# Performance work log

Hardware: AMD Instinct MI355X
Metric: run time of the kernel (lower is better)

The kernel has to match this reference:

```python
import jax, jax.numpy as jnp
import numpy as np

D_MODEL = 1024
NUM_HEADS = 16
HEAD_DIM = D_MODEL // NUM_HEADS


def setup_inputs() -> dict:
    key = jax.random.key(0)
    k_x, k_qw, k_qb, k_ow, k_ob = jax.random.split(key, 5)
    s = 1.0 / np.sqrt(D_MODEL)
    return {
        "x": jax.random.normal(k_x, (2, 2048, D_MODEL), dtype=jnp.float32),
        "qkv_w": jax.random.uniform(k_qw, (3 * D_MODEL, D_MODEL), jnp.float32, -s, s),
        "qkv_b": jax.random.uniform(k_qb, (3 * D_MODEL,), jnp.float32, -s, s),
        "out_w": jax.random.uniform(k_ow, (D_MODEL, D_MODEL), jnp.float32, -s, s),
        "out_b": jax.random.uniform(k_ob, (D_MODEL,), jnp.float32, -s, s),
    }


def reference(x, qkv_w, qkv_b, out_w, out_b):
    B, S, D = x.shape
    # fused QKV projection: [B,S,3D]
    qkv = jnp.einsum("bsd,ed->bse", x, qkv_w) + qkv_b
    # [B,S,H,3*hd] -> [B,H,S,3*hd]
    qkv = qkv.reshape(B, S, NUM_HEADS, 3 * HEAD_DIM).transpose(0, 2, 1, 3)
    q, k, v = jnp.split(qkv, 3, axis=-1)
    scale = 1.0 / jnp.sqrt(jnp.asarray(HEAD_DIM, x.dtype))
    scores = jnp.einsum("bhqd,bhkd->bhqk", q, k) * scale
    attn = jax.nn.softmax(scores, axis=-1)
    vals = jnp.einsum("bhqk,bhkd->bhqd", attn, v)
    vals = vals.transpose(0, 2, 1, 3).reshape(B, S, D)
    return jnp.einsum("bsd,ed->bse", vals, out_w) + out_b
```

## Files before the change

kernel.cpp:

```cpp
#include <hip/hip_runtime.h>
#include <stdint.h>


#define D_MODEL 1024
#define NUM_HEADS 16
#define HEAD_DIM 64
#define BATCH 2
#define SEQ 2048
#define M_TOT (BATCH * SEQ)
#define QKV_N (3 * D_MODEL)

typedef __attribute__((ext_vector_type(8))) short bf16x8;
typedef __attribute__((ext_vector_type(4))) short bf16x4;
typedef __attribute__((ext_vector_type(4))) float f32x4;
typedef __attribute__((ext_vector_type(4))) unsigned int u32x4;

__device__ __forceinline__ unsigned short f2bf(float f) {
    union { float f; unsigned int u; } v; v.f = f;
    unsigned int u = v.u;
    u += 0x7fffu + ((u >> 16) & 1u);
    return (unsigned short)(u >> 16);
}

__device__ __forceinline__ unsigned int exp2_bf16u(float x) {
    return (unsigned int)__builtin_fmaf(x, 128.0f, 16251.58f);
}

__device__ __forceinline__ unsigned int perm_pack(unsigned int hi, unsigned int lo) {
#if __has_builtin(__builtin_amdgcn_perm)
    return __builtin_amdgcn_perm(hi, lo, 0x05040100u);
#else
    return (lo & 0xFFFFu) | (hi << 16);
#endif
}

__device__ __forceinline__ void gld_lds16(const unsigned short* g,
                                          unsigned short* l) {
#if __has_builtin(__builtin_amdgcn_global_load_lds)
    __builtin_amdgcn_global_load_lds(
        (const __attribute__((address_space(1))) unsigned int*)g,
        (__attribute__((address_space(3))) unsigned int*)l, 16, 0, 0);
#else
    *(u32x4*)(l + (threadIdx.x & 63) * 8) = *(const u32x4*)g;
#endif
}

__global__ __launch_bounds__(256) void cvt_all(const float* __restrict__ x,
                                               const float* __restrict__ qw,
                                               const float* __restrict__ ow,
                                               unsigned short* __restrict__ xb,
                                               unsigned short* __restrict__ wqb,
                                               unsigned short* __restrict__ wob) {
    int i = blockIdx.x * 256 + threadIdx.x;
    const int N1 = M_TOT * D_MODEL / 8;
    const int N2 = N1 + QKV_N * D_MODEL / 8;
    const float* src; unsigned short* dst; int j;
    if (i < N1)      { src = x;  dst = xb;  j = i; }
    else if (i < N2) { src = qw; dst = wqb; j = i - N1; }
    else             { src = ow; dst = wob; j = i - N2; }
    const float4* s = (const float4*)src;
    float4 a = s[2 * j], b = s[2 * j + 1];
    u32x4 o;
    o.x = (unsigned int)f2bf(a.x) | ((unsigned int)f2bf(a.y) << 16);
    o.y = (unsigned int)f2bf(a.z) | ((unsigned int)f2bf(a.w) << 16);
    o.z = (unsigned int)f2bf(b.x) | ((unsigned int)f2bf(b.y) << 16);
    o.w = (unsigned int)f2bf(b.z) | ((unsigned int)f2bf(b.w) << 16);
    *(u32x4*)(dst + 8 * (size_t)j) = o;
}

__global__ __launch_bounds__(512, 2) void gemm_qkv(const unsigned short* __restrict__ xb,
                                                   const unsigned short* __restrict__ wb,
                                                   const float* __restrict__ bias,
                                                   unsigned short* __restrict__ qb,
                                                   unsigned short* __restrict__ kb,
                                                   unsigned short* __restrict__ vtb) {
    __shared__ __align__(16) unsigned short L[57344];

    const int tid = threadIdx.x;
    const int lane = tid & 63, wave = tid >> 6;
    const int quad = lane >> 4, l16 = lane & 15, l7 = l16 & 7;
    const int lrow = lane >> 3;
    const int sw = (lane & 7) ^ lrow;
    const int m0 = blockIdx.x * 256;
    const int n0 = blockIdx.y * 192;
    const int wmr = (wave >> 2) * 128;
    const int wn = (wave & 3) * 48;

    float biasr[3];
#pragma unroll
    for (int nt = 0; nt < 3; nt++) biasr[nt] = bias[n0 + wn + nt * 16 + l16];

    f32x4 acc[8][3];
#pragma unroll
    for (int m = 0; m < 8; m++)
#pragma unroll
        for (int nt = 0; nt < 3; nt++) acc[m][nt] = (f32x4)0.0f;

    auto stA = [&](int tt, int s, int b) {
        int R = s * 64 + wave * 8 + lrow;
        gld_lds16(xb + (size_t)(m0 + R) * D_MODEL + tt * 64 + sw * 8,
                  L + b * 16384 + (s * 64 + wave * 8) * 64);
    };
    auto stB = [&](int tt, int s, int b) {
        int R = s * 64 + wave * 8 + lrow;
        gld_lds16(wb + (size_t)(n0 + R) * D_MODEL + tt * 64 + sw * 8,
                  L + 32768 + b * 12288 + (s * 64 + wave * 8) * 64);
    };

    stB(0, 0, 0); stB(0, 1, 0); stB(0, 2, 0);
    stA(0, 0, 0); stA(0, 1, 0); stA(0, 2, 0); stA(0, 3, 0);

    const int NT = D_MODEL / 64;
    for (int t = 0; t < NT; ++t) {
        const int cb = t & 1, nb = cb ^ 1;
        const int tn = (t + 1 < NT) ? t + 1 : NT - 1;
        const unsigned short* Ac = L + cb * 16384;
        const unsigned short* Bc = L + 32768 + cb * 12288;
        bf16x8 bfr[3][2];

#pragma unroll
        for (int q = 0; q < 4; ++q) {
            if (q == 0) {
                asm volatile("s_waitcnt vmcnt(1)" ::: "memory");
                asm volatile("s_barrier" ::: "memory");
            } else if (q == 2) {
                asm volatile("s_waitcnt vmcnt(4)" ::: "memory");
                asm volatile("s_barrier" ::: "memory");
            }
            if (q == 0)      { stB(tn, 0, nb); stB(tn, 1, nb); }
            else if (q == 1) { stB(tn, 2, nb); stA(tn, 0, nb); }
            else if (q == 2) { stA(tn, 1, nb); stA(tn, 2, nb); }
            else             { stA(tn, 3, nb); }

            if (q == 0) {
#pragma unroll
                for (int nt = 0; nt < 3; nt++)
#pragma unroll
                    for (int ks = 0; ks < 2; ++ks)
                        bfr[nt][ks] = *(const bf16x8*)(
                            Bc + (wn + nt * 16 + l16) * 64 + ((ks * 4 + quad) ^ l7) * 8);
            }
            bf16x8 afr[2][2];
#pragma unroll
            for (int j = 0; j < 2; ++j)
#pragma unroll
                for (int ks = 0; ks < 2; ++ks)
                    afr[j][ks] = *(const bf16x8*)(
                        Ac + (wmr + (q * 2 + j) * 16 + l16) * 64 + ((ks * 4 + quad) ^ l7) * 8);

            __builtin_amdgcn_s_setprio(1);
#pragma unroll
            for (int j = 0; j < 2; ++j)
#pragma unroll
                for (int nt = 0; nt < 3; nt++)
#pragma unroll
                    for (int ks = 0; ks < 2; ++ks)
                        acc[q * 2 + j][nt] = __builtin_amdgcn_mfma_f32_16x16x32_bf16(
                            afr[j][ks], bfr[nt][ks], acc[q * 2 + j][nt], 0, 0, 0);
            __builtin_amdgcn_s_setprio(0);
        }
    }

    __syncthreads();

    const float QSCALE = 0.18033688011112042f;
#pragma unroll
    for (int nt = 0; nt < 3; nt++) {
        int colb = wn + nt * 16;
        int sec = colb >> 6;
        int c64 = (colb & 63) + l16;
        float bia = biasr[nt];
        if (sec < 2) {
            unsigned short* img = L + sec * 16384;
            float scl = sec ? 1.0f : QSCALE;
#pragma unroll
            for (int mt = 0; mt < 8; mt++)
#pragma unroll
                for (int r = 0; r < 4; r++) {
                    int row = wmr + mt * 16 + quad * 4 + r;
                    img[row * 64 + ((((c64 >> 3) ^ (row & 7)) << 3) | (c64 & 7))] =
                        f2bf((acc[mt][nt][r] + bia) * scl);
                }
        } else {
            unsigned short* img = L + 32768;
            int d = c64;
#pragma unroll
            for (int mt = 0; mt < 8; mt++) {
                int cs = wmr + mt * 16 + quad * 4;
                int sb = cs >> 6, c64s = cs & 63;
                unsigned short t4[4];
#pragma unroll
                for (int r = 0; r < 4; r++) t4[r] = f2bf(acc[mt][nt][r] + bia);
                *(uint64_t*)(img + (d * 4 + sb) * 64 +
                             ((((c64s >> 3) ^ (d & 7)) << 3) | (c64s & 7))) =
                    *(const uint64_t*)t4;
            }
        }
    }
    __syncthreads();

    const int bh = (m0 >> 11) * NUM_HEADS + blockIdx.y;
    const int sbase = m0 & 2047;
    const int g = lane & 7;
#pragma unroll
    for (int p = 0; p < 4; p++) {
        int rr = p * 64 + wave * 8 + (lane >> 3);
        u32x4 ch = *(const u32x4*)(L + rr * 64 + ((g ^ (rr & 7)) << 3));
        *(u32x4*)(qb + ((size_t)bh * SEQ + sbase + rr) * 64 + g * 8) = ch;
        ch = *(const u32x4*)(L + 16384 + rr * 64 + ((g ^ (rr & 7)) << 3));
        *(u32x4*)(kb + ((size_t)bh * SEQ + sbase + rr) * 64 + g * 8) = ch;
        int d = rr >> 2, sb = rr & 3;
        ch = *(const u32x4*)(L + 32768 + rr * 64 + ((g ^ (d & 7)) << 3));
        *(u32x4*)(vtb + ((size_t)bh * 64 + d) * SEQ + sbase + sb * 64 + g * 8) = ch;
    }
}

__global__ __launch_bounds__(256, 4) void attn(const unsigned short* __restrict__ qb,
                                               const unsigned short* __restrict__ kb,
                                               const unsigned short* __restrict__ vtb,
                                               unsigned short* __restrict__ vals) {
    __shared__ __align__(16) unsigned short Ks[2][64 * 64];
    __shared__ __align__(16) unsigned short VTs[2][64 * 64];

    const int tid = threadIdx.x;
    const int lane = tid & 63, wave = tid >> 6;
    const int quad = lane >> 4, l16 = lane & 15;
    const int l7 = l16 & 7;
    const int bh = blockIdx.x;
    const int q0 = blockIdx.y * 64;
    const unsigned short* qh = qb + (size_t)bh * SEQ * 64;
    const unsigned short* kh = kb + (size_t)bh * SEQ * 64;
    const unsigned short* vth = vtb + (size_t)bh * 64 * SEQ;
    const int wrow = wave * 16;

    bf16x8 aq[2];
#pragma unroll
    for (int ks = 0; ks < 2; ++ks)
        aq[ks] = *(const bf16x8*)(
            qh + (size_t)(q0 + wrow + l16) * 64 + ks * 32 + quad * 8);

    const int lrow = lane >> 3;
    const int sw = (lane & 7) ^ (lrow & 7);

    int cxl0 = ((0 * 4 + quad) ^ l7) * 8;
    int cxl1 = ((1 * 4 + quad) ^ l7) * 8;

    auto stage = [&](int t, int b) {
        int kt = t * 64;
#pragma unroll
        for (int i = 0; i < 2; ++i) {
            int R = wave * 16 + i * 8;
            int row = R + lrow;
            int krow = (row & 0x23) | ((row & 0x0C) << 1) | ((row & 0x10) >> 2);
            gld_lds16(kh + (size_t)(kt + krow) * 64 + sw * 8, &Ks[b][R * 64]);
            gld_lds16(vth + (size_t)row * SEQ + kt + sw * 8, &VTs[b][R * 64]);
        }
    };

    stage(0, 0);
    __syncthreads();

    f32x4 oacc[4];
    f32x4 lsum = (f32x4)0.0f;
#pragma unroll
    for (int nt = 0; nt < 4; nt++) oacc[nt] = (f32x4)0.0f;

    bf16x8 ones8;
#pragma unroll
    for (int j = 0; j < 8; j++) ones8[j] = (short)0x3F80;

    const int NR = SEQ / 64;
    for (int t = 0; t < NR; ++t) {
        const int cur = t & 1;
        if (t + 1 < NR) stage(t + 1, cur ^ 1);

        const unsigned short* Kc = Ks[cur];
        const unsigned short* Vc = VTs[cur];

        f32x4 sacc[4];
#pragma unroll
        for (int mk = 0; mk < 4; mk++) sacc[mk] = (f32x4)0.0f;
#pragma unroll
        for (int ks = 0; ks < 2; ++ks) {
            int cxl = ks ? cxl1 : cxl0;
            bf16x8 bk[4];
#pragma unroll
            for (int mk = 0; mk < 4; mk++)
                bk[mk] = *(const bf16x8*)(Kc + (mk * 16 + l16) * 64 + cxl);
#pragma unroll
            for (int mk = 0; mk < 4; mk++)
                sacc[mk] = __builtin_amdgcn_mfma_f32_16x16x32_bf16(
                    bk[mk], aq[ks], sacc[mk], 0, 0, 0);
        }

        bf16x4 pf[4];
#pragma unroll
        for (int mk = 0; mk < 4; mk++) {
            unsigned int u0 = exp2_bf16u(sacc[mk][0]);
            unsigned int u1 = exp2_bf16u(sacc[mk][1]);
            unsigned int u2 = exp2_bf16u(sacc[mk][2]);
            unsigned int u3 = exp2_bf16u(sacc[mk][3]);
            union { unsigned int u[2]; bf16x4 b; } cv;
            cv.u[0] = perm_pack(u1, u0);
            cv.u[1] = perm_pack(u3, u2);
            pf[mk] = cv.b;
        }

#pragma unroll
        for (int w = 0; w < 2; ++w) {
            bf16x8 ap = __builtin_shufflevector(
                pf[2 * w], pf[2 * w + 1], 0, 1, 2, 3, 4, 5, 6, 7);
            int cxl = w ? cxl1 : cxl0;
#pragma unroll
            for (int nt = 0; nt < 4; nt++) {
                bf16x8 bv = *(const bf16x8*)(Vc + (nt * 16 + l16) * 64 + cxl);
                oacc[nt] = __builtin_amdgcn_mfma_f32_16x16x32_bf16(
                    ap, bv, oacc[nt], 0, 0, 0);
            }
            lsum = __builtin_amdgcn_mfma_f32_16x16x32_bf16(
                ap, ones8, lsum, 0, 0, 0);
        }
        __syncthreads();
    }

    const int b = bh >> 4, h = bh & 15;
    f32x4 inv;
#pragma unroll
    for (int r = 0; r < 4; r++) inv[r] = 1.0f / lsum[r];
#pragma unroll
    for (int nt = 0; nt < 4; nt++) {
        int d = nt * 16 + l16;
#pragma unroll
        for (int r = 0; r < 4; r++) {
            int row = wrow + quad * 4 + r;
            float v = oacc[nt][r] * inv[r];
            vals[((size_t)(b * SEQ + q0 + row)) * D_MODEL + h * 64 + d] =
                f2bf(v);
        }
    }
}

__global__ __launch_bounds__(512, 2) void gemm_out(const unsigned short* __restrict__ vb,
                                                   const unsigned short* __restrict__ wb,
                                                   const float* __restrict__ bias,
                                                   float* __restrict__ out) {
    __shared__ __align__(16) unsigned short L[32768];

    const int tid = threadIdx.x;
    const int lane = tid & 63, wave = tid >> 6;
    const int quad = lane >> 4, l16 = lane & 15, l7 = l16 & 7;
    const int lrow = lane >> 3;
    const int sw = (lane & 7) ^ lrow;
    const int m0 = blockIdx.y * 128, n0 = blockIdx.x * 128;
    const int wm = (wave >> 2) * 64;
    const int wn = (wave & 3) * 32;

    float biasr[2];
#pragma unroll
    for (int nt = 0; nt < 2; nt++) biasr[nt] = bias[n0 + wn + nt * 16 + l16];

    f32x4 acc[4][2];
#pragma unroll
    for (int mt = 0; mt < 4; mt++)
#pragma unroll
        for (int nt = 0; nt < 2; nt++) acc[mt][nt] = (f32x4)0.0f;

    auto stA = [&](int tt, int s, int b) {
        int R = (wave >> 2) * 64 + s * 32 + (wave & 3) * 8;
        gld_lds16(vb + (size_t)(m0 + R + lrow) * D_MODEL + tt * 64 + sw * 8,
                  L + b * 8192 + R * 64);
    };
    auto stB = [&](int tt, int s, int b) {
        int R = s * 64 + wave * 8;
        gld_lds16(wb + (size_t)(n0 + R + lrow) * D_MODEL + tt * 64 + sw * 8,
                  L + 16384 + b * 8192 + R * 64);
    };

    stB(0, 0, 0); stB(0, 1, 0); stA(0, 0, 0); stA(0, 1, 0);

    const int NT = D_MODEL / 64;
    for (int t = 0; t < NT; ++t) {
        const int cb = t & 1, nb = cb ^ 1;
        const int tn = (t + 1 < NT) ? t + 1 : NT - 1;
        const unsigned short* Ac = L + cb * 8192;
        const unsigned short* Bc = L + 16384 + cb * 8192;
        bf16x8 bfr[2][2];

#pragma unroll
        for (int p = 0; p < 2; ++p) {
            if (p == 0) {
                asm volatile("s_waitcnt vmcnt(1)" ::: "memory");
                asm volatile("s_barrier" ::: "memory");
                stB(tn, 0, nb); stB(tn, 1, nb);
            } else {
                asm volatile("s_waitcnt vmcnt(2)" ::: "memory");
                asm volatile("s_barrier" ::: "memory");
                stA(tn, 0, nb); stA(tn, 1, nb);
            }

            if (p == 0) {
#pragma unroll
                for (int nt = 0; nt < 2; nt++)
#pragma unroll
                    for (int ks = 0; ks < 2; ++ks)
                        bfr[nt][ks] = *(const bf16x8*)(
                            Bc + (wn + nt * 16 + l16) * 64 + ((ks * 4 + quad) ^ l7) * 8);
            }
            bf16x8 afr[2][2];
#pragma unroll
            for (int j = 0; j < 2; ++j)
#pragma unroll
                for (int ks = 0; ks < 2; ++ks)
                    afr[j][ks] = *(const bf16x8*)(
                        Ac + (wm + (p * 2 + j) * 16 + l16) * 64 + ((ks * 4 + quad) ^ l7) * 8);

            __builtin_amdgcn_s_setprio(1);
#pragma unroll
            for (int j = 0; j < 2; ++j)
#pragma unroll
                for (int nt = 0; nt < 2; nt++)
#pragma unroll
                    for (int ks = 0; ks < 2; ++ks)
                        acc[p * 2 + j][nt] = __builtin_amdgcn_mfma_f32_16x16x32_bf16(
                            afr[j][ks], bfr[nt][ks], acc[p * 2 + j][nt], 0, 0, 0);
            __builtin_amdgcn_s_setprio(0);
        }
    }

#pragma unroll
    for (int mt = 0; mt < 4; mt++)
#pragma unroll
        for (int nt = 0; nt < 2; nt++) {
            int n = n0 + wn + nt * 16 + l16;
#pragma unroll
            for (int r = 0; r < 4; r++) {
                int m = m0 + wm + mt * 16 + quad * 4 + r;
                out[(size_t)m * D_MODEL + n] = acc[mt][nt][r] + biasr[nt];
            }
        }
}

extern "C" void kernel_launch(void* const* d_in, const int* in_sizes, int n_in,
                              void* d_out, int out_size, void* d_ws, size_t ws_size,
                              hipStream_t stream) {
    const float* x = (const float*)d_in[0];
    const float* qkv_w = (const float*)d_in[1];
    const float* qkv_b = (const float*)d_in[2];
    const float* out_w = (const float*)d_in[3];
    const float* out_b = (const float*)d_in[4];
    float* out = (float*)d_out;

    char* ws = (char*)d_ws;
    size_t off = 0;
    auto carve = [&](size_t bytes) -> void* {
        void* p = ws + off;
        off += (bytes + 255) & ~(size_t)255;
        return p;
    };
    unsigned short* xb  = (unsigned short*)carve((size_t)M_TOT * D_MODEL * 2);
    unsigned short* wqb = (unsigned short*)carve((size_t)QKV_N * D_MODEL * 2);
    unsigned short* wob = (unsigned short*)carve((size_t)D_MODEL * D_MODEL * 2);
    unsigned short* qbuf = (unsigned short*)carve((size_t)M_TOT * D_MODEL * 2);
    unsigned short* kbuf = (unsigned short*)carve((size_t)M_TOT * D_MODEL * 2);
    unsigned short* vtb  = (unsigned short*)carve((size_t)M_TOT * D_MODEL * 2);
    unsigned short* vals = xb;

    const int NCHUNK = (M_TOT + QKV_N + D_MODEL) * D_MODEL / 8;
    cvt_all<<<NCHUNK / 256, 256, 0, stream>>>(x, qkv_w, out_w, xb, wqb, wob);

    gemm_qkv<<<dim3(M_TOT / 256, QKV_N / 192), 512, 0, stream>>>(
        xb, wqb, qkv_b, qbuf, kbuf, vtb);

    attn<<<dim3(BATCH * NUM_HEADS, SEQ / 64), 256, 0, stream>>>(
        qbuf, kbuf, vtb, vals);

    gemm_out<<<dim3(D_MODEL / 128, M_TOT / 128), 512, 0, stream>>>(
        vals, wob, out_b, out);
}
```

Measured before the change: 170.5 us.

## Give each attention wave two 16-row query tiles and halve block size

The attention kernel now launches 128 threads (2 waves) per 64-query block instead of 256, and each wave handles 32 query rows as two 16-row MFMA tiles. Each K/V fragment read from LDS is reused across both query tiles, which halves LDS reads per MFMA, and each thread stages twice as many K/V rows. The cost is more accumulator registers per wave and fewer waves per block to hide latency, and the launch-bounds occupancy hint drops from 4 to 2.

```diff
diff --git a/kernel.cpp b/kernel.cpp
--- a/kernel.cpp
+++ b/kernel.cpp
@@ -215,7 +215,7 @@
     }
 }
 
-__global__ __launch_bounds__(256, 4) void attn(const unsigned short* __restrict__ qb,
+__global__ __launch_bounds__(128, 2) void attn(const unsigned short* __restrict__ qb,
                                                const unsigned short* __restrict__ kb,
                                                const unsigned short* __restrict__ vtb,
                                                unsigned short* __restrict__ vals) {
@@ -231,13 +231,15 @@
     const unsigned short* qh = qb + (size_t)bh * SEQ * 64;
     const unsigned short* kh = kb + (size_t)bh * SEQ * 64;
     const unsigned short* vth = vtb + (size_t)bh * 64 * SEQ;
-    const int wrow = wave * 16;
-
-    bf16x8 aq[2];
-#pragma unroll
-    for (int ks = 0; ks < 2; ++ks)
-        aq[ks] = *(const bf16x8*)(
-            qh + (size_t)(q0 + wrow + l16) * 64 + ks * 32 + quad * 8);
+    const int wrow = wave * 32;
+
+    bf16x8 aq[2][2];
+#pragma unroll
+    for (int nq = 0; nq < 2; nq++)
+#pragma unroll
+        for (int ks = 0; ks < 2; ++ks)
+            aq[nq][ks] = *(const bf16x8*)(
+                qh + (size_t)(q0 + wrow + nq * 16 + l16) * 64 + ks * 32 + quad * 8);
 
     const int lrow = lane >> 3;
     const int sw = (lane & 7) ^ (lrow & 7);
@@ -248,8 +250,8 @@
     auto stage = [&](int t, int b) {
         int kt = t * 64;
 #pragma unroll
-        for (int i = 0; i < 2; ++i) {
-            int R = wave * 16 + i * 8;
+        for (int i = 0; i < 4; ++i) {
+            int R = wave * 32 + i * 8;
             int row = R + lrow;
             int krow = (row & 0x23) | ((row & 0x0C) << 1) | ((row & 0x10) >> 2);
             gld_lds16(kh + (size_t)(kt + krow) * 64 + sw * 8, &Ks[b][R * 64]);
@@ -260,10 +262,14 @@
     stage(0, 0);
     __syncthreads();
 
-    f32x4 oacc[4];
-    f32x4 lsum = (f32x4)0.0f;
-#pragma unroll
-    for (int nt = 0; nt < 4; nt++) oacc[nt] = (f32x4)0.0f;
+    f32x4 oacc[2][4];
+    f32x4 lsum[2];
+#pragma unroll
+    for (int mt = 0; mt < 2; mt++) {
+        lsum[mt] = (f32x4)0.0f;
+#pragma unroll
+        for (int nt = 0; nt < 4; nt++) oacc[mt][nt] = (f32x4)0.0f;
+    }
 
     bf16x8 ones8;
 #pragma unroll
@@ -277,9 +283,11 @@
         const unsigned short* Kc = Ks[cur];
         const unsigned short* Vc = VTs[cur];
 
-        f32x4 sacc[4];
-#pragma unroll
-        for (int mk = 0; mk < 4; mk++) sacc[mk] = (f32x4)0.0f;
+        f32x4 sacc[4][2];
+#pragma unroll
+        for (int mk = 0; mk < 4; mk++)
+#pragma unroll
+            for (int nq = 0; nq < 2; nq++) sacc[mk][nq] = (f32x4)0.0f;
 #pragma unroll
         for (int ks = 0; ks < 2; ++ks) {
             int cxl = ks ? cxl1 : cxl0;
@@ -289,53 +297,66 @@
                 bk[mk] = *(const bf16x8*)(Kc + (mk * 16 + l16) * 64 + cxl);
 #pragma unroll
             for (int mk = 0; mk < 4; mk++)
-                sacc[mk] = __builtin_amdgcn_mfma_f32_16x16x32_bf16(
-                    bk[mk], aq[ks], sacc[mk], 0, 0, 0);
-        }
-
-        bf16x4 pf[4];
-#pragma unroll
-        for (int mk = 0; mk < 4; mk++) {
-            unsigned int u0 = exp2_bf16u(sacc[mk][0]);
-            unsigned int u1 = exp2_bf16u(sacc[mk][1]);
-            unsigned int u2 = exp2_bf16u(sacc[mk][2]);
-            unsigned int u3 = exp2_bf16u(sacc[mk][3]);
-            union { unsigned int u[2]; bf16x4 b; } cv;
-            cv.u[0] = perm_pack(u1, u0);
-            cv.u[1] = perm_pack(u3, u2);
-            pf[mk] = cv.b;
-        }
+#pragma unroll
+                for (int nq = 0; nq < 2; nq++)
+                    sacc[mk][nq] = __builtin_amdgcn_mfma_f32_16x16x32_bf16(
+                        bk[mk], aq[nq][ks], sacc[mk][nq], 0, 0, 0);
+        }
+
+        bf16x4 pf[4][2];
+#pragma unroll
+        for (int mk = 0; mk < 4; mk++)
+#pragma unroll
+            for (int nq = 0; nq < 2; nq++) {
+                unsigned int u0 = exp2_bf16u(sacc[mk][nq][0]);
+                unsigned int u1 = exp2_bf16u(sacc[mk][nq][1]);
+                unsigned int u2 = exp2_bf16u(sacc[mk][nq][2]);
+                unsigned int u3 = exp2_bf16u(sacc[mk][nq][3]);
+                union { unsigned int u[2]; bf16x4 b; } cv;
+                cv.u[0] = perm_pack(u1, u0);
+                cv.u[1] = perm_pack(u3, u2);
+                pf[mk][nq] = cv.b;
+            }
 
 #pragma unroll
         for (int w = 0; w < 2; ++w) {
-            bf16x8 ap = __builtin_shufflevector(
-                pf[2 * w], pf[2 * w + 1], 0, 1, 2, 3, 4, 5, 6, 7);
+            bf16x8 ap0 = __builtin_shufflevector(
+                pf[2 * w][0], pf[2 * w + 1][0], 0, 1, 2, 3, 4, 5, 6, 7);
+            bf16x8 ap1 = __builtin_shufflevector(
+                pf[2 * w][1], pf[2 * w + 1][1], 0, 1, 2, 3, 4, 5, 6, 7);
             int cxl = w ? cxl1 : cxl0;
 #pragma unroll
             for (int nt = 0; nt < 4; nt++) {
                 bf16x8 bv = *(const bf16x8*)(Vc + (nt * 16 + l16) * 64 + cxl);
-                oacc[nt] = __builtin_amdgcn_mfma_f32_16x16x32_bf16(
-                    ap, bv, oacc[nt], 0, 0, 0);
-            }
-            lsum = __builtin_amdgcn_mfma_f32_16x16x32_bf16(
-                ap, ones8, lsum, 0, 0, 0);
+                oacc[0][nt] = __builtin_amdgcn_mfma_f32_16x16x32_bf16(
+                    ap0, bv, oacc[0][nt], 0, 0, 0);
+                oacc[1][nt] = __builtin_amdgcn_mfma_f32_16x16x32_bf16(
+                    ap1, bv, oacc[1][nt], 0, 0, 0);
+            }
+            lsum[0] = __builtin_amdgcn_mfma_f32_16x16x32_bf16(
+                ap0, ones8, lsum[0], 0, 0, 0);
+            lsum[1] = __builtin_amdgcn_mfma_f32_16x16x32_bf16(
+                ap1, ones8, lsum[1], 0, 0, 0);
         }
         __syncthreads();
     }
 
     const int b = bh >> 4, h = bh & 15;
-    f32x4 inv;
-#pragma unroll
-    for (int r = 0; r < 4; r++) inv[r] = 1.0f / lsum[r];
-#pragma unroll
-    for (int nt = 0; nt < 4; nt++) {
-        int d = nt * 16 + l16;
-#pragma unroll
-        for (int r = 0; r < 4; r++) {
-            int row = wrow + quad * 4 + r;
-            float v = oacc[nt][r] * inv[r];
-            vals[((size_t)(b * SEQ + q0 + row)) * D_MODEL + h * 64 + d] =
-                f2bf(v);
+#pragma unroll
+    for (int mt = 0; mt < 2; mt++) {
+        f32x4 inv;
+#pragma unroll
+        for (int r = 0; r < 4; r++) inv[r] = 1.0f / lsum[mt][r];
+#pragma unroll
+        for (int nt = 0; nt < 4; nt++) {
+            int d = nt * 16 + l16;
+#pragma unroll
+            for (int r = 0; r < 4; r++) {
+                int row = wrow + mt * 16 + quad * 4 + r;
+                float v = oacc[mt][nt][r] * inv[r];
+                vals[((size_t)(b * SEQ + q0 + row)) * D_MODEL + h * 64 + d] =
+                    f2bf(v);
+            }
         }
     }
 }
@@ -471,7 +492,7 @@
     gemm_qkv<<<dim3(M_TOT / 256, QKV_N / 192), 512, 0, stream>>>(
         xb, wqb, qkv_b, qbuf, kbuf, vtb);
 
-    attn<<<dim3(BATCH * NUM_HEADS, SEQ / 64), 256, 0, stream>>>(
+    attn<<<dim3(BATCH * NUM_HEADS, SEQ / 64), 128, 0, stream>>>(
         qbuf, kbuf, vtb, vals);
 
     gemm_out<<<dim3(D_MODEL / 128, M_TOT / 128), 512, 0, stream>>>(
```

After: 176.1 us. 3.3% more time.

## Fuse all four stages into one persistent cooperative kernel with grid syncs

Applied to the files above, without the earlier changes.

Replaces the four launches (convert, QKV GEMM, attention, output GEMM) with a single cooperative kernel of 256 blocks of 512 threads that runs each phase in turn, separated by grid.sync. The aim is to remove launch gaps and tail effects between kernels. In exchange, each phase is now tied to a fixed 256-block grid: attention runs two 256-thread units per block over two passes, and the GEMMs are remapped onto that grid. Grid-wide barriers add their own cost, and occupancy is limited to what fits co-resident.

```diff
diff --git a/kernel.cpp b/kernel.cpp
--- a/kernel.cpp
+++ b/kernel.cpp
@@ -1,5 +1,8 @@
 #include <hip/hip_runtime.h>
+#include <hip/hip_cooperative_groups.h>
 #include <stdint.h>
+
+namespace cg = cooperative_groups;
 
 
 #define D_MODEL 1024
@@ -45,399 +48,407 @@
 #endif
 }
 
-__global__ __launch_bounds__(256) void cvt_all(const float* __restrict__ x,
-                                               const float* __restrict__ qw,
-                                               const float* __restrict__ ow,
-                                               unsigned short* __restrict__ xb,
-                                               unsigned short* __restrict__ wqb,
-                                               unsigned short* __restrict__ wob) {
-    int i = blockIdx.x * 256 + threadIdx.x;
-    const int N1 = M_TOT * D_MODEL / 8;
-    const int N2 = N1 + QKV_N * D_MODEL / 8;
-    const float* src; unsigned short* dst; int j;
-    if (i < N1)      { src = x;  dst = xb;  j = i; }
-    else if (i < N2) { src = qw; dst = wqb; j = i - N1; }
-    else             { src = ow; dst = wob; j = i - N2; }
-    const float4* s = (const float4*)src;
-    float4 a = s[2 * j], b = s[2 * j + 1];
-    u32x4 o;
-    o.x = (unsigned int)f2bf(a.x) | ((unsigned int)f2bf(a.y) << 16);
-    o.y = (unsigned int)f2bf(a.z) | ((unsigned int)f2bf(a.w) << 16);
-    o.z = (unsigned int)f2bf(b.x) | ((unsigned int)f2bf(b.y) << 16);
-    o.w = (unsigned int)f2bf(b.z) | ((unsigned int)f2bf(b.w) << 16);
-    *(u32x4*)(dst + 8 * (size_t)j) = o;
-}
-
-__global__ __launch_bounds__(512, 2) void gemm_qkv(const unsigned short* __restrict__ xb,
-                                                   const unsigned short* __restrict__ wb,
-                                                   const float* __restrict__ bias,
-                                                   unsigned short* __restrict__ qb,
-                                                   unsigned short* __restrict__ kb,
-                                                   unsigned short* __restrict__ vtb) {
+__global__ __launch_bounds__(512, 2) void mha_fused(
+        const float* __restrict__ x, const float* __restrict__ qw,
+        const float* __restrict__ ow, const float* __restrict__ qkv_bias,
+        const float* __restrict__ out_bias,
+        unsigned short* __restrict__ xb, unsigned short* __restrict__ wqb,
+        unsigned short* __restrict__ wob, unsigned short* __restrict__ qb,
+        unsigned short* __restrict__ kb, unsigned short* __restrict__ vtb,
+        float* __restrict__ out) {
     __shared__ __align__(16) unsigned short L[57344];
-
+    cg::grid_group grid = cg::this_grid();
+
+    const int b = blockIdx.x;
     const int tid = threadIdx.x;
-    const int lane = tid & 63, wave = tid >> 6;
-    const int quad = lane >> 4, l16 = lane & 15, l7 = l16 & 7;
-    const int lrow = lane >> 3;
-    const int sw = (lane & 7) ^ lrow;
-    const int m0 = blockIdx.x * 256;
-    const int n0 = blockIdx.y * 192;
-    const int wmr = (wave >> 2) * 128;
-    const int wn = (wave & 3) * 48;
-
-    float biasr[3];
-#pragma unroll
-    for (int nt = 0; nt < 3; nt++) biasr[nt] = bias[n0 + wn + nt * 16 + l16];
-
-    f32x4 acc[8][3];
-#pragma unroll
-    for (int m = 0; m < 8; m++)
-#pragma unroll
-        for (int nt = 0; nt < 3; nt++) acc[m][nt] = (f32x4)0.0f;
-
-    auto stA = [&](int tt, int s, int b) {
-        int R = s * 64 + wave * 8 + lrow;
-        gld_lds16(xb + (size_t)(m0 + R) * D_MODEL + tt * 64 + sw * 8,
-                  L + b * 16384 + (s * 64 + wave * 8) * 64);
-    };
-    auto stB = [&](int tt, int s, int b) {
-        int R = s * 64 + wave * 8 + lrow;
-        gld_lds16(wb + (size_t)(n0 + R) * D_MODEL + tt * 64 + sw * 8,
-                  L + 32768 + b * 12288 + (s * 64 + wave * 8) * 64);
-    };
-
-    stB(0, 0, 0); stB(0, 1, 0); stB(0, 2, 0);
-    stA(0, 0, 0); stA(0, 1, 0); stA(0, 2, 0); stA(0, 3, 0);
-
-    const int NT = D_MODEL / 64;
-    for (int t = 0; t < NT; ++t) {
-        const int cb = t & 1, nb = cb ^ 1;
-        const int tn = (t + 1 < NT) ? t + 1 : NT - 1;
-        const unsigned short* Ac = L + cb * 16384;
-        const unsigned short* Bc = L + 32768 + cb * 12288;
-        bf16x8 bfr[3][2];
-
-#pragma unroll
-        for (int q = 0; q < 4; ++q) {
-            if (q == 0) {
-                asm volatile("s_waitcnt vmcnt(1)" ::: "memory");
-                asm volatile("s_barrier" ::: "memory");
-            } else if (q == 2) {
-                asm volatile("s_waitcnt vmcnt(4)" ::: "memory");
-                asm volatile("s_barrier" ::: "memory");
-            }
-            if (q == 0)      { stB(tn, 0, nb); stB(tn, 1, nb); }
-            else if (q == 1) { stB(tn, 2, nb); stA(tn, 0, nb); }
-            else if (q == 2) { stA(tn, 1, nb); stA(tn, 2, nb); }
-            else             { stA(tn, 3, nb); }
-
-            if (q == 0) {
-#pragma unroll
-                for (int nt = 0; nt < 3; nt++)
+
+    {
+        const int N1 = M_TOT * D_MODEL / 8;
+        const int N2 = N1 + QKV_N * D_MODEL / 8;
+#pragma unroll
+        for (int it = 0; it < 8; ++it) {
+            int i = it * 131072 + b * 512 + tid;
+            const float* src; unsigned short* dst; int j;
+            if (i < N1)      { src = x;  dst = xb;  j = i; }
+            else if (i < N2) { src = qw; dst = wqb; j = i - N1; }
+            else             { src = ow; dst = wob; j = i - N2; }
+            const float4* s = (const float4*)src;
+            float4 a = s[2 * j], c = s[2 * j + 1];
+            u32x4 o;
+            o.x = (unsigned int)f2bf(a.x) | ((unsigned int)f2bf(a.y) << 16);
+            o.y = (unsigned int)f2bf(a.z) | ((unsigned int)f2bf(a.w) << 16);
+            o.z = (unsigned int)f2bf(c.x) | ((unsigned int)f2bf(c.y) << 16);
+            o.w = (unsigned int)f2bf(c.z) | ((unsigned int)f2bf(c.w) << 16);
+            *(u32x4*)(dst + 8 * (size_t)j) = o;
+        }
+    }
+    grid.sync();
+    asm volatile("s_waitcnt vmcnt(0) lgkmcnt(0)" ::: "memory");
+
+    {
+        const int lane = tid & 63, wave = tid >> 6;
+        const int quad = lane >> 4, l16 = lane & 15, l7 = l16 & 7;
+        const int lrow = lane >> 3;
+        const int sw = (lane & 7) ^ lrow;
+        const int m0 = (b & 15) * 256;
+        const int n0 = (b >> 4) * 192;
+        const int wmr = (wave >> 2) * 128;
+        const int wn = (wave & 3) * 48;
+
+        float biasr[3];
+#pragma unroll
+        for (int nt = 0; nt < 3; nt++) biasr[nt] = qkv_bias[n0 + wn + nt * 16 + l16];
+
+        f32x4 acc[8][3];
+#pragma unroll
+        for (int m = 0; m < 8; m++)
+#pragma unroll
+            for (int nt = 0; nt < 3; nt++) acc[m][nt] = (f32x4)0.0f;
+
+        auto stA = [&](int tt, int s, int bb) {
+            int R = s * 64 + wave * 8 + lrow;
+            gld_lds16(xb + (size_t)(m0 + R) * D_MODEL + tt * 64 + sw * 8,
+                      L + bb * 16384 + (s * 64 + wave * 8) * 64);
+        };
+        auto stB = [&](int tt, int s, int bb) {
+            int R = s * 64 + wave * 8 + lrow;
+            gld_lds16(wqb + (size_t)(n0 + R) * D_MODEL + tt * 64 + sw * 8,
+                      L + 32768 + bb * 12288 + (s * 64 + wave * 8) * 64);
+        };
+
+        stB(0, 0, 0); stB(0, 1, 0); stB(0, 2, 0);
+        stA(0, 0, 0); stA(0, 1, 0); stA(0, 2, 0); stA(0, 3, 0);
+
+        const int NT = D_MODEL / 64;
+        for (int t = 0; t < NT; ++t) {
+            const int cb = t & 1, nb = cb ^ 1;
+            const int tn = (t + 1 < NT) ? t + 1 : NT - 1;
+            const unsigned short* Ac = L + cb * 16384;
+            const unsigned short* Bc = L + 32768 + cb * 12288;
+            bf16x8 bfr[3][2];
+
+#pragma unroll
+            for (int q = 0; q < 4; ++q) {
+                if (q == 0) {
+                    asm volatile("s_waitcnt vmcnt(1)" ::: "memory");
+                    asm volatile("s_barrier" ::: "memory");
+                } else if (q == 2) {
+                    asm volatile("s_waitcnt vmcnt(4)" ::: "memory");
+                    asm volatile("s_barrier" ::: "memory");
+                }
+                if (q == 0)      { stB(tn, 0, nb); stB(tn, 1, nb); }
+                else if (q == 1) { stB(tn, 2, nb); stA(tn, 0, nb); }
+                else if (q == 2) { stA(tn, 1, nb); stA(tn, 2, nb); }
+                else             { stA(tn, 3, nb); }
+
+                if (q == 0) {
+#pragma unroll
+                    for (int nt = 0; nt < 3; nt++)
+#pragma unroll
+                        for (int ks = 0; ks < 2; ++ks)
+                            bfr[nt][ks] = *(const bf16x8*)(
+                                Bc + (wn + nt * 16 + l16) * 64 + ((ks * 4 + quad) ^ l7) * 8);
+                }
+                bf16x8 afr[2][2];
+#pragma unroll
+                for (int j = 0; j < 2; ++j)
 #pragma unroll
                     for (int ks = 0; ks < 2; ++ks)
-                        bfr[nt][ks] = *(const bf16x8*)(
-                            Bc + (wn + nt * 16 + l16) * 64 + ((ks * 4 + quad) ^ l7) * 8);
-            }
-            bf16x8 afr[2][2];
-#pragma unroll
-            for (int j = 0; j < 2; ++j)
-#pragma unroll
-                for (int ks = 0; ks < 2; ++ks)
-                    afr[j][ks] = *(const bf16x8*)(
-                        Ac + (wmr + (q * 2 + j) * 16 + l16) * 64 + ((ks * 4 + quad) ^ l7) * 8);
-
-            __builtin_amdgcn_s_setprio(1);
-#pragma unroll
-            for (int j = 0; j < 2; ++j)
-#pragma unroll
-                for (int nt = 0; nt < 3; nt++)
+                        afr[j][ks] = *(const bf16x8*)(
+                            Ac + (wmr + (q * 2 + j) * 16 + l16) * 64 + ((ks * 4 + quad) ^ l7) * 8);
+
+                __builtin_amdgcn_s_setprio(1);
+#pragma unroll
+                for (int j = 0; j < 2; ++j)
+#pragma unroll
+                    for (int nt = 0; nt < 3; nt++)
+#pragma unroll
+                        for (int ks = 0; ks < 2; ++ks)
+                            acc[q * 2 + j][nt] = __builtin_amdgcn_mfma_f32_16x16x32_bf16(
+                                afr[j][ks], bfr[nt][ks], acc[q * 2 + j][nt], 0, 0, 0);
+                __builtin_amdgcn_s_setprio(0);
+            }
+        }
+
+        __syncthreads();
+
+        const float QSCALE = 0.18033688011112042f;
+#pragma unroll
+        for (int nt = 0; nt < 3; nt++) {
+            int colb = wn + nt * 16;
+            int sec = colb >> 6;
+            int c64 = (colb & 63) + l16;
+            float bia = biasr[nt];
+            if (sec < 2) {
+                unsigned short* img = L + sec * 16384;
+                float scl = sec ? 1.0f : QSCALE;
+#pragma unroll
+                for (int mt = 0; mt < 8; mt++)
+#pragma unroll
+                    for (int r = 0; r < 4; r++) {
+                        int row = wmr + mt * 16 + quad * 4 + r;
+                        img[row * 64 + ((((c64 >> 3) ^ (row & 7)) << 3) | (c64 & 7))] =
+                            f2bf((acc[mt][nt][r] + bia) * scl);
+                    }
+            } else {
+                unsigned short* img = L + 32768;
+                int d = c64;
+#pragma unroll
+                for (int mt = 0; mt < 8; mt++) {
+                    int cs = wmr + mt * 16 + quad * 4;
+                    int sb = cs >> 6, c64s = cs & 63;
+                    unsigned short t4[4];
+#pragma unroll
+                    for (int r = 0; r < 4; r++) t4[r] = f2bf(acc[mt][nt][r] + bia);
+                    *(uint64_t*)(img + (d * 4 + sb) * 64 +
+                                 ((((c64s >> 3) ^ (d & 7)) << 3) | (c64s & 7))) =
+                        *(const uint64_t*)t4;
+                }
+            }
+        }
+        __syncthreads();
+
+        const int bh = (m0 >> 11) * NUM_HEADS + (b >> 4);
+        const int sbase = m0 & 2047;
+        const int g = lane & 7;
+#pragma unroll
+        for (int p = 0; p < 4; p++) {
+            int rr = p * 64 + wave * 8 + (lane >> 3);
+            u32x4 ch = *(const u32x4*)(L + rr * 64 + ((g ^ (rr & 7)) << 3));
+            *(u32x4*)(qb + ((size_t)bh * SEQ + sbase + rr) * 64 + g * 8) = ch;
+            ch = *(const u32x4*)(L + 16384 + rr * 64 + ((g ^ (rr & 7)) << 3));
+            *(u32x4*)(kb + ((size_t)bh * SEQ + sbase + rr) * 64 + g * 8) = ch;
+            int d = rr >> 2, sb = rr & 3;
+            ch = *(const u32x4*)(L + 32768 + rr * 64 + ((g ^ (d & 7)) << 3));
+            *(u32x4*)(vtb + ((size_t)bh * 64 + d) * SEQ + sbase + sb * 64 + g * 8) = ch;
+        }
+    }
+    grid.sync();
+    asm volatile("s_waitcnt vmcnt(0) lgkmcnt(0)" ::: "memory");
+
+    {
+        const int u = tid >> 8;
+        const int utid = tid & 255;
+        const int lane = utid & 63, wave = utid >> 6;
+        const int quad = lane >> 4, l16 = lane & 15;
+        const int l7 = l16 & 7;
+        const int bh = b & 31;
+        unsigned short* UB = L + u * 16384;
+        const unsigned short* qh = qb + (size_t)bh * SEQ * 64;
+        const unsigned short* kh = kb + (size_t)bh * SEQ * 64;
+        const unsigned short* vth = vtb + (size_t)bh * 64 * SEQ;
+        const int wrow = wave * 16;
+
+        const int lrow = lane >> 3;
+        const int sw = (lane & 7) ^ (lrow & 7);
+        int cxl0 = ((0 * 4 + quad) ^ l7) * 8;
+        int cxl1 = ((1 * 4 + quad) ^ l7) * 8;
+
+        unsigned short* vals = xb;
+
+        for (int pass = 0; pass < 2; ++pass) {
+            const int q0 = ((b >> 5) * 4 + pass * 2 + u) * 64;
+
+            bf16x8 aq[2];
+#pragma unroll
+            for (int ks = 0; ks < 2; ++ks)
+                aq[ks] = *(const bf16x8*)(
+                    qh + (size_t)(q0 + wrow + l16) * 64 + ks * 32 + quad * 8);
+
+            auto stage = [&](int t, int bsel) {
+                int kt = t * 64;
+#pragma unroll
+                for (int i = 0; i < 2; ++i) {
+                    int R = wave * 16 + i * 8;
+                    int row = R + lrow;
+                    int krow = (row & 0x23) | ((row & 0x0C) << 1) | ((row & 0x10) >> 2);
+                    gld_lds16(kh + (size_t)(kt + krow) * 64 + sw * 8,
+                              UB + bsel * 4096 + R * 64);
+                    gld_lds16(vth + (size_t)row * SEQ + kt + sw * 8,
+                              UB + 8192 + bsel * 4096 + R * 64);
+                }
+            };
+
+            stage(0, 0);
+            __syncthreads();
+
+            f32x4 oacc[4];
+            f32x4 lsum = (f32x4)0.0f;
+#pragma unroll
+            for (int nt = 0; nt < 4; nt++) oacc[nt] = (f32x4)0.0f;
+
+            bf16x8 ones8;
+#pragma unroll
+            for (int j = 0; j < 8; j++) ones8[j] = (short)0x3F80;
+
+            const int NR = SEQ / 64;
+            for (int t = 0; t < NR; ++t) {
+                const int cur = t & 1;
+                if (t + 1 < NR) stage(t + 1, cur ^ 1);
+
+                const unsigned short* Kc = UB + cur * 4096;
+                const unsigned short* Vc = UB + 8192 + cur * 4096;
+
+                f32x4 sacc[4];
+#pragma unroll
+                for (int mk = 0; mk < 4; mk++) sacc[mk] = (f32x4)0.0f;
+#pragma unroll
+                for (int ks = 0; ks < 2; ++ks) {
+                    int cxl = ks ? cxl1 : cxl0;
+                    bf16x8 bk[4];
+#pragma unroll
+                    for (int mk = 0; mk < 4; mk++)
+                        bk[mk] = *(const bf16x8*)(Kc + (mk * 16 + l16) * 64 + cxl);
+#pragma unroll
+                    for (int mk = 0; mk < 4; mk++)
+                        sacc[mk] = __builtin_amdgcn_mfma_f32_16x16x32_bf16(
+                            bk[mk], aq[ks], sacc[mk], 0, 0, 0);
+                }
+
+                bf16x4 pf[4];
+#pragma unroll
+                for (int mk = 0; mk < 4; mk++) {
+                    unsigned int u0 = exp2_bf16u(sacc[mk][0]);
+                    unsigned int u1 = exp2_bf16u(sacc[mk][1]);
+                    unsigned int u2 = exp2_bf16u(sacc[mk][2]);
+                    unsigned int u3 = exp2_bf16u(sacc[mk][3]);
+                    union { unsigned int uu[2]; bf16x4 bb; } cv;
+                    cv.uu[0] = perm_pack(u1, u0);
+                    cv.uu[1] = perm_pack(u3, u2);
+                    pf[mk] = cv.bb;
+                }
+
+#pragma unroll
+                for (int w = 0; w < 2; ++w) {
+                    bf16x8 ap = __builtin_shufflevector(
+                        pf[2 * w], pf[2 * w + 1], 0, 1, 2, 3, 4, 5, 6, 7);
+                    int cxl = w ? cxl1 : cxl0;
+#pragma unroll
+                    for (int nt = 0; nt < 4; nt++) {
+                        bf16x8 bv = *(const bf16x8*)(Vc + (nt * 16 + l16) * 64 + cxl);
+                        oacc[nt] = __builtin_amdgcn_mfma_f32_16x16x32_bf16(
+                            ap, bv, oacc[nt], 0, 0, 0);
+                    }
+                    lsum = __builtin_amdgcn_mfma_f32_16x16x32_bf16(
+                        ap, ones8, lsum, 0, 0, 0);
+                }
+                __syncthreads();
+            }
+
+            const int bb = bh >> 4, h = bh & 15;
+            f32x4 inv;
+#pragma unroll
+            for (int r = 0; r < 4; r++) inv[r] = 1.0f / lsum[r];
+#pragma unroll
+            for (int nt = 0; nt < 4; nt++) {
+                int d = nt * 16 + l16;
+#pragma unroll
+                for (int r = 0; r < 4; r++) {
+                    int row = wrow + quad * 4 + r;
+                    float v = oacc[nt][r] * inv[r];
+                    vals[((size_t)(bb * SEQ + q0 + row)) * D_MODEL + h * 64 + d] =
+                        f2bf(v);
+                }
+            }
+        }
+    }
+    grid.sync();
+    asm volatile("s_waitcnt vmcnt(0) lgkmcnt(0)" ::: "memory");
+
+    {
+        const unsigned short* vb = xb;
+        const int lane = tid & 63, wave = tid >> 6;
+        const int quad = lane >> 4, l16 = lane & 15, l7 = l16 & 7;
+        const int lrow = lane >> 3;
+        const int sw = (lane & 7) ^ lrow;
+        const int m0 = (b >> 3) * 128, n0 = (b & 7) * 128;
+        const int wm = (wave >> 2) * 64;
+        const int wn = (wave & 3) * 32;
+
+        float biasr[2];
+#pragma unroll
+        for (int nt = 0; nt < 2; nt++) biasr[nt] = out_bias[n0 + wn + nt * 16 + l16];
+
+        f32x4 acc[4][2];
+#pragma unroll
+        for (int mt = 0; mt < 4; mt++)
+#pragma unroll
+            for (int nt = 0; nt < 2; nt++) acc[mt][nt] = (f32x4)0.0f;
+
+        auto stA = [&](int tt, int s, int bb) {
+            int R = (wave >> 2) * 64 + s * 32 + (wave & 3) * 8;
+            gld_lds16(vb + (size_t)(m0 + R + lrow) * D_MODEL + tt * 64 + sw * 8,
+                      L + bb * 8192 + R * 64);
+        };
+        auto stB = [&](int tt, int s, int bb) {
+            int R = s * 64 + wave * 8;
+            gld_lds16(wob + (size_t)(n0 + R + lrow) * D_MODEL + tt * 64 + sw * 8,
+                      L + 16384 + bb * 8192 + R * 64);
+        };
+
+        stB(0, 0, 0); stB(0, 1, 0); stA(0, 0, 0); stA(0, 1, 0);
+
+        const int NT = D_MODEL / 64;
+        for (int t = 0; t < NT; ++t) {
+            const int cb = t & 1, nb = cb ^ 1;
+            const int tn = (t + 1 < NT) ? t + 1 : NT - 1;
+            const unsigned short* Ac = L + cb * 8192;
+            const unsigned short* Bc = L + 16384 + cb * 8192;
+            bf16x8 bfr[2][2];
+
+#pragma unroll
+            for (int p = 0; p < 2; ++p) {
+                if (p == 0) {
+                    asm volatile("s_waitcnt vmcnt(1)" ::: "memory");
+                    asm volatile("s_barrier" ::: "memory");
+                    stB(tn, 0, nb); stB(tn, 1, nb);
+                } else {
+                    asm volatile("s_waitcnt vmcnt(2)" ::: "memory");
+                    asm volatile("s_barrier" ::: "memory");
+                    stA(tn, 0, nb); stA(tn, 1, nb);
+                }
+
+                if (p == 0) {
+#pragma unroll
+                    for (int nt = 0; nt < 2; nt++)
+#pragma unroll
+                        for (int ks = 0; ks < 2; ++ks)
+                            bfr[nt][ks] = *(const bf16x8*)(
+                                Bc + (wn + nt * 16 + l16) * 64 + ((ks * 4 + quad) ^ l7) * 8);
+                }
+                bf16x8 afr[2][2];
+#pragma unroll
+                for (int j = 0; j < 2; ++j)
 #pragma unroll
                     for (int ks = 0; ks < 2; ++ks)
-                        acc[q * 2 + j][nt] = __builtin_amdgcn_mfma_f32_16x16x32_bf16(
-                            afr[j][ks], bfr[nt][ks], acc[q * 2 + j][nt], 0, 0, 0);
-            __builtin_amdgcn_s_setprio(0);
-        }
+                        afr[j][ks] = *(const bf16x8*)(
+                            Ac + (wm + (p * 2 + j) * 16 + l16) * 64 + ((ks * 4 + quad) ^ l7) * 8);
+
+                __builtin_amdgcn_s_setprio(1);
+#pragma unroll
+                for (int j = 0; j < 2; ++j)
+#pragma unroll
+                    for (int nt = 0; nt < 2; nt++)
+#pragma unroll
+                        for (int ks = 0; ks < 2; ++ks)
+                            acc[p * 2 + j][nt] = __builtin_amdgcn_mfma_f32_16x16x32_bf16(
+                                afr[j][ks], bfr[nt][ks], acc[p * 2 + j][nt], 0, 0, 0);
+                __builtin_amdgcn_s_setprio(0);
+            }
+        }
+
+#pragma unroll
+        for (int mt = 0; mt < 4; mt++)
+#pragma unroll
+            for (int nt = 0; nt < 2; nt++) {
+                int n = n0 + wn + nt * 16 + l16;
+#pragma unroll
+                for (int r = 0; r < 4; r++) {
+                    int m = m0 + wm + mt * 16 + quad * 4 + r;
+                    out[(size_t)m * D_MODEL + n] = acc[mt][nt][r] + biasr[nt];
+                }
+            }
     }
-
-    __syncthreads();
-
-    const float QSCALE = 0.18033688011112042f;
-#pragma unroll
-    for (int nt = 0; nt < 3; nt++) {
-        int colb = wn + nt * 16;
-        int sec = colb >> 6;
-        int c64 = (colb & 63) + l16;
-        float bia = biasr[nt];
-        if (sec < 2) {
-            unsigned short* img = L + sec * 16384;
-            float scl = sec ? 1.0f : QSCALE;
-#pragma unroll
-            for (int mt = 0; mt < 8; mt++)
-#pragma unroll
-                for (int r = 0; r < 4; r++) {
-                    int row = wmr + mt * 16 + quad * 4 + r;
-                    img[row * 64 + ((((c64 >> 3) ^ (row & 7)) << 3) | (c64 & 7))] =
-                        f2bf((acc[mt][nt][r] + bia) * scl);
-                }
-        } else {
-            unsigned short* img = L + 32768;
-            int d = c64;
-#pragma unroll
-            for (int mt = 0; mt < 8; mt++) {
-                int cs = wmr + mt * 16 + quad * 4;
-                int sb = cs >> 6, c64s = cs & 63;
-                unsigned short t4[4];
-#pragma unroll
-                for (int r = 0; r < 4; r++) t4[r] = f2bf(acc[mt][nt][r] + bia);
-                *(uint64_t*)(img + (d * 4 + sb) * 64 +
-                             ((((c64s >> 3) ^ (d & 7)) << 3) | (c64s & 7))) =
-                    *(const uint64_t*)t4;
-            }
-        }
-    }
-    __syncthreads();
-
-    const int bh = (m0 >> 11) * NUM_HEADS + blockIdx.y;
-    const int sbase = m0 & 2047;
-    const int g = lane & 7;
-#pragma unroll
-    for (int p = 0; p < 4; p++) {
-        int rr = p * 64 + wave * 8 + (lane >> 3);
-        u32x4 ch = *(const u32x4*)(L + rr * 64 + ((g ^ (rr & 7)) << 3));
-        *(u32x4*)(qb + ((size_t)bh * SEQ + sbase + rr) * 64 + g * 8) = ch;
-        ch = *(const u32x4*)(L + 16384 + rr * 64 + ((g ^ (rr & 7)) << 3));
-        *(u32x4*)(kb + ((size_t)bh * SEQ + sbase + rr) * 64 + g * 8) = ch;
-        int d = rr >> 2, sb = rr & 3;
-        ch = *(const u32x4*)(L + 32768 + rr * 64 + ((g ^ (d & 7)) << 3));
-        *(u32x4*)(vtb + ((size_t)bh * 64 + d) * SEQ + sbase + sb * 64 + g * 8) = ch;
-    }
-}
-
-__global__ __launch_bounds__(256, 4) void attn(const unsigned short* __restrict__ qb,
-                                               const unsigned short* __restrict__ kb,
-                                               const unsigned short* __restrict__ vtb,
-                                               unsigned short* __restrict__ vals) {
-    __shared__ __align__(16) unsigned short Ks[2][64 * 64];
-    __shared__ __align__(16) unsigned short VTs[2][64 * 64];
-
-    const int tid = threadIdx.x;
-    const int lane = tid & 63, wave = tid >> 6;
-    const int quad = lane >> 4, l16 = lane & 15;
-    const int l7 = l16 & 7;
-    const int bh = blockIdx.x;
-    const int q0 = blockIdx.y * 64;
-    const unsigned short* qh = qb + (size_t)bh * SEQ * 64;
-    const unsigned short* kh = kb + (size_t)bh * SEQ * 64;
-    const unsigned short* vth = vtb + (size_t)bh * 64 * SEQ;
-    const int wrow = wave * 16;
-
-    bf16x8 aq[2];
-#pragma unroll
-    for (int ks = 0; ks < 2; ++ks)
-        aq[ks] = *(const bf16x8*)(
-            qh + (size_t)(q0 + wrow + l16) * 64 + ks * 32 + quad * 8);
-
-    const int lrow = lane >> 3;
-    const int sw = (lane & 7) ^ (lrow & 7);
-
-    int cxl0 = ((0 * 4 + quad) ^ l7) * 8;
-    int cxl1 = ((1 * 4 + quad) ^ l7) * 8;
-
-    auto stage = [&](int t, int b) {
-        int kt = t * 64;
-#pragma unroll
-        for (int i = 0; i < 2; ++i) {
-            int R = wave * 16 + i * 8;
-            int row = R + lrow;
-            int krow = (row & 0x23) | ((row & 0x0C) << 1) | ((row & 0x10) >> 2);
-            gld_lds16(kh + (size_t)(kt + krow) * 64 + sw * 8, &Ks[b][R * 64]);
-            gld_lds16(vth + (size_t)row * SEQ + kt + sw * 8, &VTs[b][R * 64]);
-        }
-    };
-
-    stage(0, 0);
-    __syncthreads();
-
-    f32x4 oacc[4];
-    f32x4 lsum = (f32x4)0.0f;
-#pragma unroll
-    for (int nt = 0; nt < 4; nt++) oacc[nt] = (f32x4)0.0f;
-
-    bf16x8 ones8;
-#pragma unroll
-    for (int j = 0; j < 8; j++) ones8[j] = (short)0x3F80;
-
-    const int NR = SEQ / 64;
-    for (int t = 0; t < NR; ++t) {
-        const int cur = t & 1;
-        if (t + 1 < NR) stage(t + 1, cur ^ 1);
-
-        const unsigned short* Kc = Ks[cur];
-        const unsigned short* Vc = VTs[cur];
-
-        f32x4 sacc[4];
-#pragma unroll
-        for (int mk = 0; mk < 4; mk++) sacc[mk] = (f32x4)0.0f;
-#pragma unroll
-        for (int ks = 0; ks < 2; ++ks) {
-            int cxl = ks ? cxl1 : cxl0;
-            bf16x8 bk[4];
-#pragma unroll
-            for (int mk = 0; mk < 4; mk++)
-                bk[mk] = *(const bf16x8*)(Kc + (mk * 16 + l16) * 64 + cxl);
-#pragma unroll
-            for (int mk = 0; mk < 4; mk++)
-                sacc[mk] = __builtin_amdgcn_mfma_f32_16x16x32_bf16(
-                    bk[mk], aq[ks], sacc[mk], 0, 0, 0);
-        }
-
-        bf16x4 pf[4];
-#pragma unroll
-        for (int mk = 0; mk < 4; mk++) {
-            unsigned int u0 = exp2_bf16u(sacc[mk][0]);
-            unsigned int u1 = exp2_bf16u(sacc[mk][1]);
-            unsigned int u2 = exp2_bf16u(sacc[mk][2]);
-            unsigned int u3 = exp2_bf16u(sacc[mk][3]);
-            union { unsigned int u[2]; bf16x4 b; } cv;
-            cv.u[0] = perm_pack(u1, u0);
-            cv.u[1] = perm_pack(u3, u2);
-            pf[mk] = cv.b;
-        }
-
-#pragma unroll
-        for (int w = 0; w < 2; ++w) {
-            bf16x8 ap = __builtin_shufflevector(
-                pf[2 * w], pf[2 * w + 1], 0, 1, 2, 3, 4, 5, 6, 7);
-            int cxl = w ? cxl1 : cxl0;
-#pragma unroll
-            for (int nt = 0; nt < 4; nt++) {
-                bf16x8 bv = *(const bf16x8*)(Vc + (nt * 16 + l16) * 64 + cxl);
-                oacc[nt] = __builtin_amdgcn_mfma_f32_16x16x32_bf16(
-                    ap, bv, oacc[nt], 0, 0, 0);
-            }
-            lsum = __builtin_amdgcn_mfma_f32_16x16x32_bf16(
-                ap, ones8, lsum, 0, 0, 0);
-        }
-        __syncthreads();
-    }
-
-    const int b = bh >> 4, h = bh & 15;
-    f32x4 inv;
-#pragma unroll
-    for (int r = 0; r < 4; r++) inv[r] = 1.0f / lsum[r];
-#pragma unroll
-    for (int nt = 0; nt < 4; nt++) {
-        int d = nt * 16 + l16;
-#pragma unroll
-        for (int r = 0; r < 4; r++) {
-            int row = wrow + quad * 4 + r;
-            float v = oacc[nt][r] * inv[r];
-            vals[((size_t)(b * SEQ + q0 + row)) * D_MODEL + h * 64 + d] =
-                f2bf(v);
-        }
-    }
-}
-
-__global__ __launch_bounds__(512, 2) void gemm_out(const unsigned short* __restrict__ vb,
-                                                   const unsigned short* __restrict__ wb,
-                                                   const float* __restrict__ bias,
-                                                   float* __restrict__ out) {
-    __shared__ __align__(16) unsigned short L[32768];
-
-    const int tid = threadIdx.x;
-    const int lane = tid & 63, wave = tid >> 6;
-    const int quad = lane >> 4, l16 = lane & 15, l7 = l16 & 7;
-    const int lrow = lane >> 3;
-    const int sw = (lane & 7) ^ lrow;
-    const int m0 = blockIdx.y * 128, n0 = blockIdx.x * 128;
-    const int wm = (wave >> 2) * 64;
-    const int wn = (wave & 3) * 32;
-
-    float biasr[2];
-#pragma unroll
-    for (int nt = 0; nt < 2; nt++) biasr[nt] = bias[n0 + wn + nt * 16 + l16];
-
-    f32x4 acc[4][2];
-#pragma unroll
-    for (int mt = 0; mt < 4; mt++)
-#pragma unroll
-        for (int nt = 0; nt < 2; nt++) acc[mt][nt] = (f32x4)0.0f;
-
-    auto stA = [&](int tt, int s, int b) {
-        int R = (wave >> 2) * 64 + s * 32 + (wave & 3) * 8;
-        gld_lds16(vb + (size_t)(m0 + R + lrow) * D_MODEL + tt * 64 + sw * 8,
-                  L + b * 8192 + R * 64);
-    };
-    auto stB = [&](int tt, int s, int b) {
-        int R = s * 64 + wave * 8;
-        gld_lds16(wb + (size_t)(n0 + R + lrow) * D_MODEL + tt * 64 + sw * 8,
-                  L + 16384 + b * 8192 + R * 64);
-    };
-
-    stB(0, 0, 0); stB(0, 1, 0); stA(0, 0, 0); stA(0, 1, 0);
-
-    const int NT = D_MODEL / 64;
-    for (int t = 0; t < NT; ++t) {
-        const int cb = t & 1, nb = cb ^ 1;
-        const int tn = (t + 1 < NT) ? t + 1 : NT - 1;
-        const unsigned short* Ac = L + cb * 8192;
-        const unsigned short* Bc = L + 16384 + cb * 8192;
-        bf16x8 bfr[2][2];
-
-#pragma unroll
-        for (int p = 0; p < 2; ++p) {
-            if (p == 0) {
-                asm volatile("s_waitcnt vmcnt(1)" ::: "memory");
-                asm volatile("s_barrier" ::: "memory");
-                stB(tn, 0, nb); stB(tn, 1, nb);
-            } else {
-                asm volatile("s_waitcnt vmcnt(2)" ::: "memory");
-                asm volatile("s_barrier" ::: "memory");
-                stA(tn, 0, nb); stA(tn, 1, nb);
-            }
-
-            if (p == 0) {
-#pragma unroll
-                for (int nt = 0; nt < 2; nt++)
-#pragma unroll
-                    for (int ks = 0; ks < 2; ++ks)
-                        bfr[nt][ks] = *(const bf16x8*)(
-                            Bc + (wn + nt * 16 + l16) * 64 + ((ks * 4 + quad) ^ l7) * 8);
-            }
-            bf16x8 afr[2][2];
-#pragma unroll
-            for (int j = 0; j < 2; ++j)
-#pragma unroll
-                for (int ks = 0; ks < 2; ++ks)
-                    afr[j][ks] = *(const bf16x8*)(
-                        Ac + (wm + (p * 2 + j) * 16 + l16) * 64 + ((ks * 4 + quad) ^ l7) * 8);
-
-            __builtin_amdgcn_s_setprio(1);
-#pragma unroll
-            for (int j = 0; j < 2; ++j)
-#pragma unroll
-                for (int nt = 0; nt < 2; nt++)
-#pragma unroll
-                    for (int ks = 0; ks < 2; ++ks)
-                        acc[p * 2 + j][nt] = __builtin_amdgcn_mfma_f32_16x16x32_bf16(
-                            afr[j][ks], bfr[nt][ks], acc[p * 2 + j][nt], 0, 0, 0);
-            __builtin_amdgcn_s_setprio(0);
-        }
-    }
-
-#pragma unroll
-    for (int mt = 0; mt < 4; mt++)
-#pragma unroll
-        for (int nt = 0; nt < 2; nt++) {
-            int n = n0 + wn + nt * 16 + l16;
-#pragma unroll
-            for (int r = 0; r < 4; r++) {
-                int m = m0 + wm + mt * 16 + quad * 4 + r;
-                out[(size_t)m * D_MODEL + n] = acc[mt][nt][r] + biasr[nt];
-            }
-        }
 }
 
 extern "C" void kernel_launch(void* const* d_in, const int* in_sizes, int n_in,
@@ -463,17 +474,12 @@
     unsigned short* qbuf = (unsigned short*)carve((size_t)M_TOT * D_MODEL * 2);
     unsigned short* kbuf = (unsigned short*)carve((size_t)M_TOT * D_MODEL * 2);
     unsigned short* vtb  = (unsigned short*)carve((size_t)M_TOT * D_MODEL * 2);
-    unsigned short* vals = xb;
-
-    const int NCHUNK = (M_TOT + QKV_N + D_MODEL) * D_MODEL / 8;
-    cvt_all<<<NCHUNK / 256, 256, 0, stream>>>(x, qkv_w, out_w, xb, wqb, wob);
-
-    gemm_qkv<<<dim3(M_TOT / 256, QKV_N / 192), 512, 0, stream>>>(
-        xb, wqb, qkv_b, qbuf, kbuf, vtb);
-
-    attn<<<dim3(BATCH * NUM_HEADS, SEQ / 64), 256, 0, stream>>>(
-        qbuf, kbuf, vtb, vals);
-
-    gemm_out<<<dim3(D_MODEL / 128, M_TOT / 128), 512, 0, stream>>>(
-        vals, wob, out_b, out);
-}
+
+    void* args[] = {
+        (void*)&x, (void*)&qkv_w, (void*)&out_w, (void*)&qkv_b, (void*)&out_b,
+        (void*)&xb, (void*)&wqb, (void*)&wob, (void*)&qbuf, (void*)&kbuf,
+        (void*)&vtb, (void*)&out,
+    };
+    hipLaunchCooperativeKernel((const void*)mha_fused, dim3(256), dim3(512),
+                               args, 0, stream);
+}
```

After: 286.0 us. 67.7% more time.
